# Kernel tuning notes

Hardware: AMD Instinct MI355X
Metric: run time of the kernel (lower is better)

## Reference

```python
import jax, jax.numpy as jnp
import numpy as np

KS, AS = 13, 12  # kernel_size (12 vertices + center), anchor_size (icosahedron vertices)


def _icosa():
    # Icosahedron oriented with vertex 0 on +z (required by sort_level_vs xy-rotation logic)
    r5 = np.sqrt(5.0); rr = 2.0 / r5
    vs = [[0.0, 0.0, 1.0]]
    for k in range(5):
        t = 2.0 * np.pi * k / 5.0
        vs.append([rr * np.cos(t), rr * np.sin(t), 1.0 / r5])
    for k in range(5):
        t = 2.0 * np.pi * k / 5.0 + np.pi / 5.0
        vs.append([rr * np.cos(t), rr * np.sin(t), -1.0 / r5])
    vs.append([0.0, 0.0, -1.0])
    return np.array(vs)


def _rotm(axis, ang):
    a = np.asarray(axis, dtype=np.float64); a = a / np.linalg.norm(a)
    K = np.array([[0, -a[2], a[1]], [a[2], 0, -a[0]], [-a[1], a[0], 0]])
    return np.eye(3) + np.sin(ang) * K + (1.0 - np.cos(ang)) * (K @ K)


def _ico_group(vs):
    # Generate the 60-element icosahedral rotation group by closure from two generators
    gens = [_rotm([0.0, 0.0, 1.0], 2 * np.pi / 5), _rotm(vs[1], 2 * np.pi / 5)]
    group = [np.eye(3)]
    keys = {tuple(np.round(np.eye(3), 4).ravel())}
    frontier = [np.eye(3)]
    while frontier:
        nxt = []
        for g in frontier:
            for h in gens:
                c = h @ g
                k = tuple(np.round(c, 4).ravel())
                if k not in keys:
                    keys.add(k); group.append(c); nxt.append(c)
        frontier = nxt
    return group


def _sort_level_vs(v_idxs, vs):
    # Faithful port of sort_level_vs: order ring vertices by successive 72-deg xy rotations
    out = [v_idxs[0]]
    vs_l = vs[v_idxs][:, :2]
    cur = vs_l[[0]]
    dth = 2 * np.pi / 5
    R = np.array([[np.cos(dth), -np.sin(dth)], [np.sin(dth), np.cos(dth)]])
    for _ in range(4):
        cur = R.dot(cur.T).T
        out.append(v_idxs[np.argmin(np.abs(vs_l - cur).sum(1))])
    return np.array(out)


def _build_buffers():
    vs = _icosa()
    dots = vs @ vs.T
    v0_adjs = np.where(np.abs(dots[0] - 1.0 / np.sqrt(5)) < 1e-6)[0]
    v0_lv2 = np.where(np.abs(dots[0] + 1.0 / np.sqrt(5)) < 1e-6)[0]
    v0_opp = int(np.argmin(dots[0]))
    # 12 rotation anchors: one group element mapping vertex 0 to each vertex
    group = _ico_group(vs)
    vRs = []
    for i in range(12):
        for R in group:
            if np.linalg.norm(R @ vs[0] - vs[i]) < 1e-5:
                vRs.append(R); break
    vRs = np.stack(vRs)  # [12,3,3]
    rot_v = np.einsum('rij,aj->rai', vRs, vs)  # [12,12,3]
    d = np.linalg.norm(rot_v[:, :, None, :] - vs[None, None], axis=-1)
    trace_idx_ori = np.argmin(d, axis=2)  # [12,12] vertex permutation per anchor rotation
    trace_idx_rot = np.empty_like(trace_idx_ori)
    for r in range(12):
        trace_idx_rot[r, trace_idx_ori[r]] = np.arange(12)
    trace_idxv_rot = np.concatenate([trace_idx_rot, np.full((12, 1), 12, np.int64)], axis=1)  # [12,13]
    # idx_map: faithful port of the __init__ construction (maps 13*12 slots -> 36 weight params)
    inv = np.empty(12, np.int64)
    inv[0] = 0; inv[v0_adjs] = 1; inv[v0_lv2] = 2; inv[v0_opp] = 3
    a_s = _sort_level_vs(v0_adjs, vs)
    l_s = _sort_level_vs(v0_lv2, vs)
    idx_map = np.empty(KS * AS, np.int64)
    idx_map[:AS] = inv
    idx_map[v0_opp * AS:(v0_opp + 1) * AS] = inv + 4
    idx_map[-AS:] = inv + 8
    seq1 = np.arange(12, 24); seq2 = np.arange(24, 36)
    idx_map[a_s[0] * AS:(a_s[0] + 1) * AS] = seq1
    idx_map[l_s[0] * AS:(l_s[0] + 1) * AS] = seq2
    shifts = [[4, 0, 1, 2, 3], [3, 4, 0, 1, 2], [2, 3, 4, 0, 1], [1, 2, 3, 4, 0]]
    for j, sh in enumerate(shifts, start=1):
        new = np.empty(12, np.int64)
        new[a_s] = a_s[sh]; new[l_s] = l_s[sh]
        new[0] = 0; new[v0_opp] = v0_opp
        idx_map[a_s[j] * AS:(a_s[j] + 1) * AS] = seq1[new]
        idx_map[l_s[j] * AS:(l_s[j] + 1) * AS] = seq2[new]
    return idx_map, trace_idxv_rot, trace_idx_rot


def setup_inputs() -> dict:
    key = jax.random.key(0)
    k1, k2 = jax.random.split(key)
    B, CIN, COUT, P = 8, 16, 16, 4096
    x = jax.random.normal(k1, (B, CIN, KS, P, AS), dtype=jnp.float32)
    W = jax.random.normal(k2, (COUT, CIN, 36), dtype=jnp.float32) * 0.05  # xavier-scale
    idx_map, tivr, tir = _build_buffers()
    return {
        'x': x,
        'W': W,
        'idx_map': jnp.asarray(idx_map, jnp.int32),
        'trace_idxv_rot': jnp.asarray(tivr, jnp.int32),
        'trace_idx_rot': jnp.asarray(tir, jnp.int32),
    }


def reference(x, W, idx_map, trace_idxv_rot, trace_idx_rot):
    d_out, d_in, _ = W.shape
    # Expand 36 free params to the [d, c, k, a] kernel via idx_map gather
    Wm = W[:, :, idx_map].reshape(d_out, d_in, KS, AS)
    # The two torch.gather calls (dims 2 then 3) collapse to:
    # Wfull[d,c,k,a,r] = Wm[d,c, trace_idxv_rot[r,k], trace_idx_rot[r,a]]
    Wfull = Wm[:, :, trace_idxv_rot[:, :, None], trace_idx_rot[:, None, :]]  # [d,c,r,k,a]
    return jnp.einsum('dcrka,bckpa->bdpr', Wfull, x)
```

## Files before the change

kernel.cpp:

```cpp
#include <hip/hip_runtime.h>

#define B_    8
#define CIN_  16
#define COUT_ 16
#define KS_   13
#define AS_   12
#define P_    4096
#define R_    12
#define M_    192
#define KTOT  2496
#define BN    128
#define KT    96
#define NSTEP 26
#define LDP   104

typedef float  f32x4  __attribute__((ext_vector_type(4)));
typedef __bf16 bf16x4 __attribute__((ext_vector_type(4)));
typedef __bf16 bf16x8 __attribute__((ext_vector_type(8)));

__global__ void build_wmat(const float* __restrict__ W,
                           const int* __restrict__ idx_map,
                           const int* __restrict__ tivr,
                           const int* __restrict__ tir,
                           __bf16* __restrict__ Wmat) {
  int m = blockIdx.x;
  int d = m / R_;
  int r = m - d * R_;
  for (int kap = threadIdx.x; kap < KTOT; kap += blockDim.x) {
    int c = kap / (KS_ * AS_);
    int t = kap - c * (KS_ * AS_);
    int k = t / AS_;
    int a = t - k * AS_;
    int s = idx_map[tivr[r * KS_ + k] * AS_ + tir[r * AS_ + a]];
    Wmat[m * KTOT + kap] = (__bf16)W[(d * CIN_ + c) * 36 + s];
  }
}

__global__ __launch_bounds__(512, 2)
void s2conv(const float* __restrict__ x,
            const __bf16* __restrict__ Wmat,
            float* __restrict__ out) {
  __shared__ __bf16 Ws[M_][LDP];
  __shared__ __bf16 Xs[BN][LDP];

  const int tid  = threadIdx.x;
  const int lane = tid & 63;
  const int wave = tid >> 6;
  const int wm   = wave >> 2;
  const int wn   = wave & 3;
  const int l15  = lane & 15;
  const int l4   = lane >> 4;

  const int wg = blockIdx.x;
  const int b  = wg >> 5;
  const int p0 = (wg & 31) << 7;

  f32x4  st[6];
  bf16x8 wst[5];

  f32x4 acc[6][2];
#pragma unroll
  for (int i = 0; i < 6; ++i)
#pragma unroll
    for (int j = 0; j < 2; ++j)
      acc[i][j] = f32x4{0.f, 0.f, 0.f, 0.f};

  auto load_x = [&](int kt) {
    int ck = kt * 8 + wave;
    const f32x4* bp =
        (const f32x4*)(x + (size_t)(b * 208 + ck) * 49152 + (size_t)p0 * 12);
#pragma unroll
    for (int it = 0; it < 6; ++it) st[it] = bp[it * 64 + lane];
  };

  auto load_w = [&](int kt) {
    const char* wb = (const char*)Wmat + (size_t)kt * (KT * 2);
#pragma unroll
    for (int j = 0; j < 5; ++j) {
      int i = tid + j * 512;
      if (i < 2304) {
        int row = i / 12;
        int chunk = i - row * 12;
        wst[j] = *(const bf16x8*)(wb + (size_t)row * (KTOT * 2) + chunk * 16);
      }
    }
  };

  auto write_tiles = [&]() {
#pragma unroll
    for (int j = 0; j < 5; ++j) {
      int i = tid + j * 512;
      if (i < 2304) {
        int row = i / 12;
        int chunk = i - row * 12;
        *(bf16x8*)((char*)&Ws[0][0] + row * (LDP * 2) + chunk * 16) = wst[j];
      }
    }
#pragma unroll
    for (int it = 0; it < 6; ++it) {
      int f4i = it * 64 + lane;
      int pl  = f4i / 3;
      int a   = (f4i - pl * 3) * 4;
      bf16x4 v = __builtin_convertvector(st[it], bf16x4);
      *(bf16x4*)((char*)&Xs[0][0] + pl * (LDP * 2) + (wave * 12 + a) * 2) = v;
    }
  };

  auto mfma_step = [&]() {
#pragma unroll
    for (int ks = 0; ks < 3; ++ks) {
      const int col = ks * 32 + l4 * 8;
      bf16x8 af[6], bfr[2];
#pragma unroll
      for (int mt = 0; mt < 6; ++mt)
        af[mt] = *(const bf16x8*)&Ws[wm * 96 + mt * 16 + l15][col];
#pragma unroll
      for (int nt = 0; nt < 2; ++nt)
        bfr[nt] = *(const bf16x8*)&Xs[wn * 32 + nt * 16 + l15][col];
#pragma unroll
      for (int mt = 0; mt < 6; ++mt)
#pragma unroll
        for (int nt = 0; nt < 2; ++nt)
          acc[mt][nt] = __builtin_amdgcn_mfma_f32_16x16x32_bf16(
              af[mt], bfr[nt], acc[mt][nt], 0, 0, 0);
    }
  };

  load_x(0);
  load_w(0);
  for (int kt = 0; kt < NSTEP; ++kt) {
    __syncthreads();
    write_tiles();
    __syncthreads();
    if (kt + 1 < NSTEP) {
      load_x(kt + 1);
      load_w(kt + 1);
    }
    mfma_step();
  }

#pragma unroll
  for (int mt = 0; mt < 6; ++mt) {
    int mrow0 = wm * 96 + mt * 16 + l4 * 4;
    int d  = mrow0 / 12;
    int r0 = mrow0 - d * 12;
#pragma unroll
    for (int nt = 0; nt < 2; ++nt) {
      int p = p0 + wn * 32 + nt * 16 + l15;
      float* dst = out + (size_t)((b * 16 + d) * 4096 + p) * 12 + r0;
      *(f32x4*)dst = acc[mt][nt];
    }
  }
}

extern "C" void kernel_launch(void* const* d_in, const int* in_sizes, int n_in,
                              void* d_out, int out_size, void* d_ws, size_t ws_size,
                              hipStream_t stream) {
  const float* x       = (const float*)d_in[0];
  const float* W       = (const float*)d_in[1];
  const int*   idx_map = (const int*)d_in[2];
  const int*   tivr    = (const int*)d_in[3];
  const int*   tir     = (const int*)d_in[4];
  float*       out     = (float*)d_out;
  __bf16*      Wmat    = (__bf16*)d_ws;

  build_wmat<<<dim3(M_), dim3(256), 0, stream>>>(W, idx_map, tivr, tir, Wmat);
  s2conv<<<dim3(256), dim3(512), 0, stream>>>(x, Wmat, out);
}
```

Measured before the change: 84.25 us.

## Double-buffer register prefetch two K-steps ahead with lighter barriers

Global loads of the x and W tiles are now staged in two register sets (A/B), prefetching two K-steps ahead. The loop is unrolled by two. The full __syncthreads calls are replaced by raw s_barrier, plus an LDS-only waitcnt before the second barrier, so outstanding global loads for the other buffer can stay in flight across barriers. This aims to hide HBM latency in this bandwidth-heavy GEMM. In exchange it adds about 44 VGPRs under a tight launch bound of 512 threads with 2 blocks per CU, which risks spills or reduced occupancy.

```diff
diff --git a/kernel.cpp b/kernel.cpp
--- a/kernel.cpp
+++ b/kernel.cpp
@@ -55,9 +55,6 @@
   const int b  = wg >> 5;
   const int p0 = (wg & 31) << 7;
 
-  f32x4  st[6];
-  bf16x8 wst[5];
-
   f32x4 acc[6][2];
 #pragma unroll
   for (int i = 0; i < 6; ++i)
@@ -65,7 +62,7 @@
     for (int j = 0; j < 2; ++j)
       acc[i][j] = f32x4{0.f, 0.f, 0.f, 0.f};
 
-  auto load_x = [&](int kt) {
+  auto load_x = [&](int kt, f32x4 (&st)[6]) {
     int ck = kt * 8 + wave;
     const f32x4* bp =
         (const f32x4*)(x + (size_t)(b * 208 + ck) * 49152 + (size_t)p0 * 12);
@@ -73,7 +70,7 @@
     for (int it = 0; it < 6; ++it) st[it] = bp[it * 64 + lane];
   };
 
-  auto load_w = [&](int kt) {
+  auto load_w = [&](int kt, bf16x8 (&wst)[5]) {
     const char* wb = (const char*)Wmat + (size_t)kt * (KT * 2);
 #pragma unroll
     for (int j = 0; j < 5; ++j) {
@@ -86,7 +83,7 @@
     }
   };
 
-  auto write_tiles = [&]() {
+  auto write_tiles = [&](f32x4 (&st)[6], bf16x8 (&wst)[5]) {
 #pragma unroll
     for (int j = 0; j < 5; ++j) {
       int i = tid + j * 512;
@@ -126,16 +123,29 @@
     }
   };
 
-  load_x(0);
-  load_w(0);
-  for (int kt = 0; kt < NSTEP; ++kt) {
-    __syncthreads();
-    write_tiles();
-    __syncthreads();
-    if (kt + 1 < NSTEP) {
-      load_x(kt + 1);
-      load_w(kt + 1);
-    }
+  auto barrier1 = [&]() { __builtin_amdgcn_s_barrier(); };
+  auto barrier2 = [&]() {
+    asm volatile("s_waitcnt lgkmcnt(0)" ::: "memory");
+    __builtin_amdgcn_s_barrier();
+    __builtin_amdgcn_sched_barrier(0);
+  };
+
+  f32x4  stA[6], stB[6];
+  bf16x8 wstA[5], wstB[5];
+  load_x(0, stA); load_w(0, wstA);
+  load_x(1, stB); load_w(1, wstB);
+
+  for (int kt = 0; kt < NSTEP; kt += 2) {
+    barrier1();
+    write_tiles(stA, wstA);
+    barrier2();
+    if (kt + 2 < NSTEP) { load_x(kt + 2, stA); load_w(kt + 2, wstA); }
+    mfma_step();
+
+    barrier1();
+    write_tiles(stB, wstB);
+    barrier2();
+    if (kt + 3 < NSTEP) { load_x(kt + 3, stB); load_w(kt + 3, wstB); }
     mfma_step();
   }
 
```

Result: faster. 82.58 us (-2.0%).
